# Kernel optimization log

Hardware: AMD Instinct MI355X
Metric: run time of the kernel (lower is better)

Reference implementation:

```python
import jax, jax.numpy as jnp
import numpy as np

INPUT_DIM = 256
OUTPUT_DIM = 256
DEGREE = 7


def setup_inputs() -> dict:
    key = jax.random.key(0)
    k1, k2 = jax.random.split(key)
    x = jax.random.normal(k1, (16, 2048, INPUT_DIM), dtype=jnp.float32)
    std = 1.0 / (INPUT_DIM * (DEGREE + 1))
    hermite_coeffs = std * jax.random.normal(k2, (INPUT_DIM, OUTPUT_DIM, DEGREE + 1), dtype=jnp.float32)
    return {"x": x, "hermite_coeffs": hermite_coeffs}


def reference(x, hermite_coeffs):
    a, b, c = x.shape
    degree = hermite_coeffs.shape[2] - 1
    xf = jnp.tanh(x.reshape(-1, c))  # [N, input_dim]
    hs = [jnp.ones_like(xf)]
    if degree > 0:
        hs.append(2.0 * xf)
    for i in range(2, degree + 1):
        hs.append(2.0 * xf * hs[-1] - 2.0 * (i - 1) * hs[-2])
    hermite = jnp.stack(hs, axis=-1)  # [N, input_dim, degree+1]
    y = jnp.einsum('bid,iod->bo', hermite, hermite_coeffs)
    return y.reshape(a, b, hermite_coeffs.shape[1])
```

## Files before the change

kernel.cpp:

```cpp
#include <hip/hip_runtime.h>
#include <hip/hip_bf16.h>
#include <math.h>

#define INPUT_DIM 256
#define OUT_DIM   256
#define NDEG      8
#define KTOT      (INPUT_DIM * NDEG)
#define NROWS     (16 * 2048)

#define BM  64
#define BN  128
#define BK  64
#define NK  (KTOT / BK)
#define LDT 72

typedef __bf16 bf16x8 __attribute__((ext_vector_type(8)));
typedef float  f32x4  __attribute__((ext_vector_type(4)));

__global__ __launch_bounds__(256) void reorder_coeffs(const float* __restrict__ C,
                                                      __bf16* __restrict__ Bt) {
    int g = blockIdx.x * 256 + threadIdx.x;
    int i = g >> 8;
    int o = g & 255;
    const float4* src = (const float4*)(C + (size_t)i * (OUT_DIM * NDEG) + o * NDEG);
    float4 a = src[0];
    float4 b = src[1];
    bf16x8 v;
    v[0] = (__bf16)a.x; v[1] = (__bf16)a.y; v[2] = (__bf16)a.z; v[3] = (__bf16)a.w;
    v[4] = (__bf16)b.x; v[5] = (__bf16)b.y; v[6] = (__bf16)b.z; v[7] = (__bf16)b.w;
    *(bf16x8*)(Bt + (size_t)o * KTOT + i * NDEG) = v;
}

__global__ __launch_bounds__(256, 4) void hermite_mfma(const float* __restrict__ x,
                                                       const __bf16* __restrict__ Bt,
                                                       float* __restrict__ out) {
    __shared__ __align__(16) __bf16 Alds[BM * LDT];
    __shared__ __align__(16) __bf16 Blds[BN * LDT];

    const int tid  = threadIdx.x;
    const int bm   = blockIdx.x;
    const int bn   = blockIdx.y;
    const int wave = tid >> 6;
    const int lane = tid & 63;
    const int wr   = (wave >> 1) * 32;
    const int wc   = (wave & 1) * 64;
    const int lrow = lane & 15;
    const int quad = lane >> 4;

    const int am = tid >> 2;
    const int ah = (tid & 3) * 2;
    const float* xrow = x + (size_t)(bm * BM + am) * INPUT_DIM + ah;

    const int bo   = tid >> 3;
    const int bseg = (tid & 7) * 8;
    const __bf16* bbase = Bt + (size_t)(bn * BN + bo) * KTOT + bseg;

    f32x4 acc[2][4] = {};

    for (int kc = 0; kc < NK; ++kc) {
        uint4 bv0 = *(const uint4*)(bbase + (size_t)0 * 32 * KTOT + kc * BK);
        uint4 bv1 = *(const uint4*)(bbase + (size_t)1 * 32 * KTOT + kc * BK);
        uint4 bv2 = *(const uint4*)(bbase + (size_t)2 * 32 * KTOT + kc * BK);
        uint4 bv3 = *(const uint4*)(bbase + (size_t)3 * 32 * KTOT + kc * BK);
        float2 xv = *(const float2*)(xrow + kc * 8);

        #pragma unroll
        for (int j = 0; j < 2; ++j) {
            float xs = (&xv.x)[j];
            float e = __expf(2.0f * xs);
            float t = 1.0f - 2.0f / (e + 1.0f);
            bf16x8 v;
            float hm2 = 1.0f;
            float hm1 = 2.0f * t;
            v[0] = (__bf16)hm2;
            v[1] = (__bf16)hm1;
            #pragma unroll
            for (int d = 2; d < 8; ++d) {
                float h = 2.0f * t * hm1 - 2.0f * (float)(d - 1) * hm2;
                v[d] = (__bf16)h;
                hm2 = hm1; hm1 = h;
            }
            *(bf16x8*)(&Alds[am * LDT + (ah + j) * 8]) = v;
        }

        *(uint4*)(&Blds[(bo +  0) * LDT + bseg]) = bv0;
        *(uint4*)(&Blds[(bo + 32) * LDT + bseg]) = bv1;
        *(uint4*)(&Blds[(bo + 64) * LDT + bseg]) = bv2;
        *(uint4*)(&Blds[(bo + 96) * LDT + bseg]) = bv3;

        __syncthreads();

        #pragma unroll
        for (int ki = 0; ki < 2; ++ki) {
            bf16x8 af[2], bfr[4];
            #pragma unroll
            for (int mi = 0; mi < 2; ++mi)
                af[mi] = *(const bf16x8*)(&Alds[(wr + mi * 16 + lrow) * LDT + ki * 32 + quad * 8]);
            #pragma unroll
            for (int ni = 0; ni < 4; ++ni)
                bfr[ni] = *(const bf16x8*)(&Blds[(wc + ni * 16 + lrow) * LDT + ki * 32 + quad * 8]);
            #pragma unroll
            for (int mi = 0; mi < 2; ++mi)
                #pragma unroll
                for (int ni = 0; ni < 4; ++ni)
                    acc[mi][ni] = __builtin_amdgcn_mfma_f32_16x16x32_bf16(
                        af[mi], bfr[ni], acc[mi][ni], 0, 0, 0);
        }

        __syncthreads();
    }

    #pragma unroll
    for (int mi = 0; mi < 2; ++mi) {
        #pragma unroll
        for (int r = 0; r < 4; ++r) {
            int row = bm * BM + wr + mi * 16 + quad * 4 + r;
            float* orow = out + (size_t)row * OUT_DIM + bn * BN + wc + lrow;
            #pragma unroll
            for (int ni = 0; ni < 4; ++ni)
                orow[ni * 16] = acc[mi][ni][r];
        }
    }
}

extern "C" void kernel_launch(void* const* d_in, const int* in_sizes, int n_in,
                              void* d_out, int out_size, void* d_ws, size_t ws_size,
                              hipStream_t stream) {
    const float* x = (const float*)d_in[0];
    const float* C = (const float*)d_in[1];
    float* out = (float*)d_out;
    __bf16* Bt = (__bf16*)d_ws;

    reorder_coeffs<<<dim3((INPUT_DIM * OUT_DIM) / 256), dim3(256), 0, stream>>>(C, Bt);
    hermite_mfma<<<dim3(NROWS / BM, OUT_DIM / BN), dim3(256), 0, stream>>>(x, Bt, out);
}
```

Before: 134.1 us.

## Load coefficient tiles directly into LDS with pre-chunked global layout

Reorders the bf16 coefficient workspace into contiguous per-tile chunks of 8192 elements, laid out by k-group then output column. The main kernel then copies each chunk straight into shared memory with global_load_lds, bypassing registers. This removes the VGPR round trip and the separate LDS stores for B, and adjusts the fragment read indexing to the new unpadded layout. The unpadded layout may bring LDS bank conflicts, and it relies on the barrier waiting for the asynchronous loads.

```diff
diff --git a/kernel.cpp b/kernel.cpp
--- a/kernel.cpp
+++ b/kernel.cpp
@@ -13,6 +13,7 @@
 #define BK  64
 #define NK  (KTOT / BK)
 #define LDT 72
+#define CHUNK_ELEMS 8192
 
 typedef __bf16 bf16x8 __attribute__((ext_vector_type(8)));
 typedef float  f32x4  __attribute__((ext_vector_type(4)));
@@ -28,14 +29,19 @@
     bf16x8 v;
     v[0] = (__bf16)a.x; v[1] = (__bf16)a.y; v[2] = (__bf16)a.z; v[3] = (__bf16)a.w;
     v[4] = (__bf16)b.x; v[5] = (__bf16)b.y; v[6] = (__bf16)b.z; v[7] = (__bf16)b.w;
-    *(bf16x8*)(Bt + (size_t)o * KTOT + i * NDEG) = v;
+    int bn = o >> 7;
+    int ol = o & 127;
+    int kc = i >> 3;
+    int p  = i & 7;
+    size_t dst = (size_t)(bn * 32 + kc) * CHUNK_ELEMS + p * 1024 + ol * 8;
+    *(bf16x8*)(Bt + dst) = v;
 }
 
 __global__ __launch_bounds__(256, 4) void hermite_mfma(const float* __restrict__ x,
                                                        const __bf16* __restrict__ Bt,
                                                        float* __restrict__ out) {
     __shared__ __align__(16) __bf16 Alds[BM * LDT];
-    __shared__ __align__(16) __bf16 Blds[BN * LDT];
+    __shared__ __align__(16) __bf16 Blds[CHUNK_ELEMS];
 
     const int tid  = threadIdx.x;
     const int bm   = blockIdx.x;
@@ -51,18 +57,22 @@
     const int ah = (tid & 3) * 2;
     const float* xrow = x + (size_t)(bm * BM + am) * INPUT_DIM + ah;
 
-    const int bo   = tid >> 3;
-    const int bseg = (tid & 7) * 8;
-    const __bf16* bbase = Bt + (size_t)(bn * BN + bo) * KTOT + bseg;
+    const __bf16* chunk0 = Bt + (size_t)bn * 32 * CHUNK_ELEMS;
+    const int woff = wave * 2048 + lane * 8;
 
     f32x4 acc[2][4] = {};
 
     for (int kc = 0; kc < NK; ++kc) {
-        uint4 bv0 = *(const uint4*)(bbase + (size_t)0 * 32 * KTOT + kc * BK);
-        uint4 bv1 = *(const uint4*)(bbase + (size_t)1 * 32 * KTOT + kc * BK);
-        uint4 bv2 = *(const uint4*)(bbase + (size_t)2 * 32 * KTOT + kc * BK);
-        uint4 bv3 = *(const uint4*)(bbase + (size_t)3 * 32 * KTOT + kc * BK);
         float2 xv = *(const float2*)(xrow + kc * 8);
+
+        const __bf16* gsrc = chunk0 + (size_t)kc * CHUNK_ELEMS + woff;
+        #pragma unroll
+        for (int i = 0; i < 4; ++i) {
+            __builtin_amdgcn_global_load_lds(
+                (const __attribute__((address_space(1))) void*)(gsrc + i * 512),
+                (__attribute__((address_space(3))) void*)(&Blds[wave * 2048 + i * 512 + lane * 8]),
+                16, 0, 0);
+        }
 
         #pragma unroll
         for (int j = 0; j < 2; ++j) {
@@ -83,11 +93,6 @@
             *(bf16x8*)(&Alds[am * LDT + (ah + j) * 8]) = v;
         }
 
-        *(uint4*)(&Blds[(bo +  0) * LDT + bseg]) = bv0;
-        *(uint4*)(&Blds[(bo + 32) * LDT + bseg]) = bv1;
-        *(uint4*)(&Blds[(bo + 64) * LDT + bseg]) = bv2;
-        *(uint4*)(&Blds[(bo + 96) * LDT + bseg]) = bv3;
-
         __syncthreads();
 
         #pragma unroll
@@ -98,7 +103,7 @@
                 af[mi] = *(const bf16x8*)(&Alds[(wr + mi * 16 + lrow) * LDT + ki * 32 + quad * 8]);
             #pragma unroll
             for (int ni = 0; ni < 4; ++ni)
-                bfr[ni] = *(const bf16x8*)(&Blds[(wc + ni * 16 + lrow) * LDT + ki * 32 + quad * 8]);
+                bfr[ni] = *(const bf16x8*)(&Blds[((ki * 4 + quad) * 128 + (wc + ni * 16 + lrow)) * 8]);
             #pragma unroll
             for (int mi = 0; mi < 2; ++mi)
                 #pragma unroll
```

Measured after the change: 123.9 us. 1.08x faster.
